# Optimization experiments

Measured on AMD Instinct MI355X. Metric: run time of the kernel, lower is better.

Reference implementation:

```python
import jax, jax.numpy as jnp
import numpy as np

SR = 8                      # search_range
MO = 2 * SR + 1             # max_offset = 17
NC = MO * MO                # 289 cost-volume channels


def _l2_normalize(x, eps=1e-12):
    # torch F.normalize(p=2, dim=1): x / max(||x||_2, eps)
    n = jnp.sqrt(jnp.sum(x * x, axis=1, keepdims=True))
    return x / jnp.maximum(n, eps)


def _conv2d(x, w, b, pad, groups=1):
    out = jax.lax.conv_general_dilated(
        x, w, window_strides=(1, 1), padding=[(pad, pad), (pad, pad)],
        feature_group_count=groups,
        dimension_numbers=('NCHW', 'OIHW', 'NCHW'))
    return out + b[None, :, None, None]


def _cost_volume(x1, x2, sr, norm_both=False):
    x1 = _l2_normalize(x1)
    if norm_both:
        x2 = _l2_normalize(x2)
    bs, c, h, w = x1.shape
    padded = jnp.pad(x2, ((0, 0), (0, 0), (sr, sr), (sr, sr)))
    mo = 2 * sr + 1
    # offsets in (j outer, i inner) order, matching the original double loop
    jj, ii = jnp.meshgrid(jnp.arange(mo), jnp.arange(mo), indexing='ij')
    offs = jnp.stack([jj.reshape(-1), ii.reshape(-1)], axis=-1)  # [mo^2, 2]

    def step(carry, off):
        sl = jax.lax.dynamic_slice(padded, (0, 0, off[0], off[1]), (bs, c, h, w))
        return carry, jnp.mean(x1 * sl, axis=1)  # [bs, h, w]

    _, cv = jax.lax.scan(step, None, offs)       # [mo^2, bs, h, w]
    cv = jnp.transpose(cv, (1, 0, 2, 3))          # [bs, mo^2, h, w]
    return jax.nn.leaky_relu(cv, 0.1)


def setup_inputs() -> dict:
    key = jax.random.key(0)
    ks = jax.random.split(key, 8)
    bs, c, h, w = 4, 256, 64, 64
    scale = 0.05
    return {
        'f1': jax.random.normal(ks[0], (bs, c, h, w), jnp.float32),
        'f2': jax.random.normal(ks[1], (bs, c, h, w), jnp.float32),
        'att_w': jax.random.normal(ks[2], (NC, 1, 7, 7), jnp.float32) * scale,
        'att_b': jax.random.normal(ks[3], (NC,), jnp.float32) * scale,
        'agg1_w': jax.random.normal(ks[4], (NC // 2, NC, 3, 3), jnp.float32) * scale,
        'agg1_b': jax.random.normal(ks[5], (NC // 2,), jnp.float32) * scale,
        'agg2_w': jax.random.normal(ks[6], (49, NC // 2, 3, 3), jnp.float32) * scale,
        'agg2_b': jax.random.normal(ks[7], (49,), jnp.float32) * scale,
    }


def reference(f1, f2, att_w, att_b, agg1_w, agg1_b, agg2_w, agg2_b):
    match_vol = _cost_volume(f1, f2, SR, norm_both=False)          # [bs,289,h,w]
    att = _conv2d(match_vol, att_w, att_b, pad=3, groups=NC)       # depthwise 7x7
    att_vol = match_vol * att
    h1 = jax.nn.relu(_conv2d(att_vol, agg1_w, agg1_b, pad=1))      # Conv(289->144,3)
    out = jax.nn.relu(_conv2d(h1, agg2_w, agg2_b, pad=1))          # Conv(144->49,3)
    return out
```

## Files before the change

### kernel.cpp

```cpp
#include <hip/hip_runtime.h>
#include <hip/hip_bf16.h>

#define BS   4
#define C    256
#define HW   4096
#define NPIX 16384
#define NCH  289
#define MO   17
#define PH   80
#define PW   80
#define C1   144
#define C2   49
#define ASTR 264
#define ICP  320
#define IC3  192
#define CVP  70
#define CVC  320
#define CH64 72

typedef __bf16  bf16x8 __attribute__((ext_vector_type(8)));
typedef float   f32x4  __attribute__((ext_vector_type(4)));
typedef unsigned short us8 __attribute__((ext_vector_type(8)));

__device__ __forceinline__ void halo_zero_dev(unsigned short* p, int H, int halo,
                                              int Cc, int blk, int t) {
    int W = H;
    int inter = H - 2 * halo;
    int total_pos = H * W - inter * inter;
    int chunks = Cc >> 3;
    size_t tot = (size_t)total_pos * chunks * BS;
    size_t idx = (size_t)blk * 256 + t;
    if (idx >= tot) return;
    int c8 = (int)(idx % chunks);
    size_t r = idx / chunks;
    int pos = (int)(r % total_pos);
    int b = (int)(r / total_pos);
    int h, w;
    int topbot = 2 * halo * W;
    if (pos < halo * W) { h = pos / W; w = pos % W; }
    else if (pos < topbot) { int q = pos - halo * W; h = H - halo + q / W; w = q % W; }
    else {
        int q = pos - topbot;
        int row = q / (2 * halo), off = q % (2 * halo);
        h = halo + row;
        w = (off < halo) ? off : (W - 2 * halo + off);
    }
    us8 z = {0, 0, 0, 0, 0, 0, 0, 0};
    *(us8*)&p[(((size_t)b * H + h) * W + w) * Cc + c8 * 8] = z;
}

__global__ void setup_kernel(unsigned short* __restrict__ x2bf, unsigned short* __restrict__ cvp,
                             unsigned short* __restrict__ avp, unsigned short* __restrict__ h1p,
                             const float* __restrict__ w1, unsigned short* __restrict__ wb1,
                             const float* __restrict__ w2, unsigned short* __restrict__ wb2,
                             const float* __restrict__ att_w, float* __restrict__ wdwp,
                             const float* __restrict__ f1, unsigned short* __restrict__ x1bf,
                             const float* __restrict__ f2) {
    __shared__ float shmem[16 * 257 + 16];
    int blk = blockIdx.x;
    int t = threadIdx.x;
    if (blk < 4030) {
        if (blk < 1152) { halo_zero_dev(x2bf, PH, 8, C, blk, t); return; }
        if (blk < 1655) { halo_zero_dev(cvp, CVP, 3, CVC, blk - 1152, t); return; }
        if (blk < 1818) { halo_zero_dev(avp, 66, 1, ICP, blk - 1655, t); return; }
        if (blk < 1916) { halo_zero_dev(h1p, 66, 1, IC3, blk - 1818, t); return; }
        if (blk < 3536) {
            int idx = (blk - 1916) * 256 + t;
            int tap = idx / (C1 * ICP);
            int r = idx - tap * (C1 * ICP);
            int oc = r / ICP;
            int ic = r - oc * ICP;
            float v = (ic < NCH) ? w1[((size_t)(oc * NCH + ic)) * 9 + tap] : 0.f;
            __hip_bfloat16 hb = __float2bfloat16(v);
            wb1[idx] = *(unsigned short*)&hb;
            return;
        }
        if (blk < 3968) {
            int idx = (blk - 3536) * 256 + t;
            int tap = idx / (64 * IC3);
            int r = idx - tap * (64 * IC3);
            int oc = r / IC3;
            int ic = r - oc * IC3;
            float v = (oc < C2 && ic < C1) ? w2[((size_t)(oc * C1 + ic)) * 9 + tap] : 0.f;
            __hip_bfloat16 hb = __float2bfloat16(v);
            wb2[idx] = *(unsigned short*)&hb;
            return;
        }
        {
            int idx = (blk - 3968) * 256 + t;
            if (idx >= 49 * CVC) return;
            int tap = idx / CVC;
            int ch = idx - tap * CVC;
            wdwp[idx] = (ch < NCH) ? att_w[ch * 49 + tap] : 0.f;
        }
        return;
    }
    if (blk < 5054) {
        float* tileT = shmem;
        float* invS = shmem + 16 * 257;
        int bb = blk - 4030;
        int pblk = bb & 255, b = bb >> 8;
        int p0 = pblk * 16;
        int tx = t & 15, ty = t >> 4;
        const float* s = f1 + (size_t)b * C * HW;
#pragma unroll
        for (int i2 = 0; i2 < 16; ++i2) {
            int c = ty + 16 * i2;
            tileT[tx * 257 + c] = s[(size_t)c * HW + p0 + tx];
        }
        __syncthreads();
        int px = t >> 4;
        int l = t & 15;
        float ssum = 0.f;
#pragma unroll
        for (int j2 = 0; j2 < 16; ++j2) {
            float v = tileT[px * 257 + l + 16 * j2];
            ssum += v * v;
        }
        ssum += __shfl_xor(ssum, 1);
        ssum += __shfl_xor(ssum, 2);
        ssum += __shfl_xor(ssum, 4);
        ssum += __shfl_xor(ssum, 8);
        if (l == 0) invS[px] = 1.0f / fmaxf(sqrtf(ssum), 1e-12f);
        __syncthreads();
#pragma unroll 4
        for (int p = 0; p < 16; ++p) {
            float v = tileT[p * 257 + t] * invS[p];
            __hip_bfloat16 hb = __float2bfloat16(v);
            x1bf[((size_t)b * HW + p0 + p) * C + t] = *(unsigned short*)&hb;
        }
        return;
    }
    {
        float* tile = shmem;
        int bb = blk - 5054;
        int pblk = bb & 127;
        int cblk = (bb >> 7) & 7;
        int b    = bb >> 10;
        int tx = t & 31, ty = t >> 5;
        int c0 = cblk * 32, p0 = pblk * 32;
        const float* s = f2 + (size_t)b * C * HW;
#pragma unroll
        for (int i = 0; i < 4; ++i) {
            int c = c0 + ty + 8 * i;
            tile[(ty + 8 * i) * 33 + tx] = s[(size_t)c * HW + p0 + tx];
        }
        __syncthreads();
#pragma unroll
        for (int i = 0; i < 4; ++i) {
            int p = p0 + ty + 8 * i;
            float v = tile[tx * 33 + ty + 8 * i];
            int c = c0 + tx;
            int h = p >> 6, w = p & 63;
            __hip_bfloat16 hb = __float2bfloat16(v);
            x2bf[(((size_t)b * PH + h + 8) * PW + (w + 8)) * C + c] = *(unsigned short*)&hb;
        }
    }
}

__global__ __launch_bounds__(512, 2)
void cv_mfma_kernel(const unsigned short* __restrict__ x1b,
                    const unsigned short* __restrict__ x2b,
                    unsigned short* __restrict__ cvp) {
    __shared__ __align__(16) unsigned short x2s[2][32 * ASTR];
    int i = blockIdx.x;
    int xcd = i & 7;
    int j = i >> 3;
    int hp = xcd * 2 + (j & 1);
    int jj = j >> 1;
    int wseg = jj & 3;
    int b = jj >> 2;
    int h0 = hp * 4;
    int w0 = wseg * 16;
    int t = threadIdx.x;
    int wave = t >> 6, lane = t & 63;
    int lrow = lane & 15, quad = lane >> 4;
    int row_w = wave >> 1, ct = wave & 1;
    int h = h0 + row_w;
    int col_l = ct * 16 + lrow;

    const unsigned short* x1p = x1b + ((size_t)b * HW + h * 64 + w0) * C;
    bf16x8 a[8];
#pragma unroll
    for (int kk = 0; kk < 8; ++kk)
        a[kk] = *(const bf16x8*)&x1p[(size_t)lrow * C + kk * 32 + quad * 8];

    const unsigned short* x2base = x2b + (size_t)b * PH * PW * C;

    {
        const unsigned short* rowp = x2base + ((size_t)h0 * PW + w0) * C;
#pragma unroll
        for (int s = 0; s < 2; ++s) {
            int v = t + s * 512;
            int col = v >> 5, ch8 = v & 31;
            *(us8*)&x2s[0][col * ASTR + ch8 * 8] = *(const us8*)&rowp[(size_t)col * C + ch8 * 8];
        }
    }
    __syncthreads();

    for (int rr = 0; rr < 20; ++rr) {
        us8 pr[2];
        bool dop = (rr + 1 < 20);
        if (dop) {
            const unsigned short* rowp = x2base + ((size_t)(h0 + rr + 1) * PW + w0) * C;
#pragma unroll
            for (int s = 0; s < 2; ++s) {
                int v = t + s * 512;
                int col = v >> 5, ch8 = v & 31;
                pr[s] = *(const us8*)&rowp[(size_t)col * C + ch8 * 8];
            }
        }

        int dj = rr - row_w;
        if ((unsigned)dj <= 16u) {
            const unsigned short* xs = x2s[rr & 1];
            f32x4 acc = {0.f, 0.f, 0.f, 0.f};
#pragma unroll
            for (int kk = 0; kk < 8; ++kk) {
                bf16x8 bb = *(const bf16x8*)&xs[col_l * ASTR + kk * 32 + quad * 8];
                acc = __builtin_amdgcn_mfma_f32_16x16x32_bf16(a[kk], bb, acc, 0, 0, 0);
            }
#pragma unroll
            for (int r = 0; r < 4; ++r) {
                int px_l = quad * 4 + r;
                int di = col_l - px_l;
                if ((unsigned)di <= 16u) {
                    float v = acc[r] * (1.0f / 256.0f);
                    v = (v > 0.f) ? v : 0.1f * v;
                    __hip_bfloat16 hb = __float2bfloat16(v);
                    cvp[(((size_t)b * CVP + h + 3) * CVP + (w0 + px_l + 3)) * CVC + dj * MO + di] =
                        *(unsigned short*)&hb;
                }
            }
        }

        if (dop) {
            unsigned short* dst = x2s[(rr + 1) & 1];
#pragma unroll
            for (int s = 0; s < 2; ++s) {
                int v = t + s * 512;
                int col = v >> 5, ch8 = v & 31;
                *(us8*)&dst[col * ASTR + ch8 * 8] = pr[s];
            }
            __syncthreads();
        }
    }
}

__global__ __launch_bounds__(256, 4)
void dw_att_tiled(const unsigned short* __restrict__ cvp,
                  const float* __restrict__ wdwp,
                  const float* __restrict__ att_b, unsigned short* __restrict__ av_pad) {
    __shared__ __align__(16) unsigned short actS[14 * 14 * 64];
    __shared__ float wdwS[49 * 64];
    int i = blockIdx.x;
    int ty = i & 7;
    int j = i >> 3;
    int cc = j % 5;
    int rest = j / 5;
    int tx = rest & 7, b = rest >> 3;
    int x0 = tx * 8, y0 = ty * 8;
    int c0 = cc * 64;
    int t = threadIdx.x;

    const unsigned short* cvb = cvp + (((size_t)b * CVP + y0) * CVP + x0) * CVC + c0;
    for (int v = t; v < 14 * 14 * 8; v += 256) {
        int rc = v >> 3, c8v = v & 7;
        int yy = rc / 14, xx = rc - yy * 14;
        *(us8*)&actS[rc * 64 + c8v * 8] =
            *(const us8*)&cvb[((size_t)yy * CVP + xx) * CVC + c8v * 8];
    }
    for (int v = t; v < 49 * 64; v += 256) {
        int tap = v >> 6, ch = v & 63;
        wdwS[v] = wdwp[tap * CVC + c0 + ch];
    }
    __syncthreads();

    int pr2 = t & 31;
    int rowg = t >> 5;
    int chl0 = 2 * pr2;
    int ch0 = c0 + chl0;
    float bv0 = (ch0 < NCH) ? att_b[ch0] : 0.f;
    float bv1 = (ch0 + 1 < NCH) ? att_b[ch0 + 1] : 0.f;
    float acc0[8], acc1[8];
#pragma unroll
    for (int px = 0; px < 8; ++px) { acc0[px] = bv0; acc1[px] = bv1; }

    for (int dy = 0; dy < 7; ++dy) {
        float w0[7], w1[7];
#pragma unroll
        for (int dx = 0; dx < 7; ++dx) {
            float2 wv = *(const float2*)&wdwS[(dy * 7 + dx) * 64 + chl0];
            w0[dx] = wv.x; w1[dx] = wv.y;
        }
        int row = rowg + dy;
        float r0[14], r1[14];
#pragma unroll
        for (int xx = 0; xx < 14; ++xx) {
            unsigned u = *(const unsigned*)&actS[(row * 14 + xx) * 64 + chl0];
            r0[xx] = __uint_as_float(u << 16);
            r1[xx] = __uint_as_float(u & 0xffff0000u);
        }
#pragma unroll
        for (int dx = 0; dx < 7; ++dx)
#pragma unroll
            for (int px = 0; px < 8; ++px) {
                acc0[px] += r0[px + dx] * w0[dx];
                acc1[px] += r1[px + dx] * w1[dx];
            }
    }

    if (ch0 < NCH) {
        bool pair = (ch0 + 1 < NCH);
#pragma unroll
        for (int px = 0; px < 8; ++px) {
            unsigned u = *(const unsigned*)&actS[((rowg + 3) * 14 + (px + 3)) * 64 + chl0];
            float c0v = __uint_as_float(u << 16);
            float c1v = __uint_as_float(u & 0xffff0000u);
            __hip_bfloat16 h0 = __float2bfloat16(c0v * acc0[px]);
            __hip_bfloat16 h1 = __float2bfloat16(c1v * acc1[px]);
            size_t o = (((size_t)b * 66 + y0 + rowg + 1) * 66 + (x0 + px + 1)) * ICP + ch0;
            if (pair) {
                unsigned ov = ((unsigned)*(unsigned short*)&h1 << 16) | (unsigned)*(unsigned short*)&h0;
                *(unsigned*)&av_pad[o] = ov;
            } else {
                av_pad[o] = *(unsigned short*)&h0;
            }
        }
    }
}

__global__ void agg1_mfma_kernel(const unsigned short* __restrict__ av_pad,
                                 const unsigned short* __restrict__ wb1,
                                 const float* __restrict__ bias,
                                 unsigned short* __restrict__ h1p) {
    __shared__ __align__(16) unsigned short aS2[2][66 * CH64];
    int i = blockIdx.x;
    int xcd = i & 7;
    int j = i >> 3;
    int h = xcd * 8 + (j & 7);
    int b = j >> 3;
    int t = threadIdx.x;
    int wave = t >> 6, lane = t & 63;
    int lrow = lane & 15, quad = lane >> 4;
    int ot0 = (wave == 0) ? 0 : (wave * 2 + 1);
    int nt  = (wave == 0) ? 3 : 2;

    f32x4 acc[4][3];
#pragma unroll
    for (int m = 0; m < 4; ++m)
#pragma unroll
        for (int ii = 0; ii < 3; ++ii) acc[m][ii] = (f32x4){0.f, 0.f, 0.f, 0.f};

    const unsigned short* avb = av_pad + (((size_t)b * 66 + h) * 66) * ICP;

    {
        const unsigned short* arow = avb;
        *(us8*)&aS2[0][(t >> 3) * CH64 + (t & 7) * 8] =
            *(const us8*)&arow[(size_t)(t >> 3) * ICP + (t & 7) * 8];
        {
            int v = t + 256;
            *(us8*)&aS2[0][(v >> 3) * CH64 + (v & 7) * 8] =
                *(const us8*)&arow[(size_t)(v >> 3) * ICP + (v & 7) * 8];
        }
        if (t < 16) {
            int v = t + 512;
            *(us8*)&aS2[0][(v >> 3) * CH64 + (v & 7) * 8] =
                *(const us8*)&arow[(size_t)(v >> 3) * ICP + (v & 7) * 8];
        }
    }
    bf16x8 bcur[3][2], bnxt[3][2];
#pragma unroll
    for (int ii = 0; ii < 3; ++ii)
        if (ii < nt)
#pragma unroll
            for (int c2 = 0; c2 < 2; ++c2)
                bcur[ii][c2] = *(const bf16x8*)&wb1[((size_t)((ot0 + ii) * 16 + lrow)) * ICP +
                                                    c2 * 32 + quad * 8];
    __syncthreads();

    for (int p2 = 0; p2 < 15; ++p2) {
        int dy = p2 / 5, cc = p2 % 5;
        us8 ar0, ar1, ar2;
        bool doA = (p2 + 1 < 15);
        if (doA) {
            int dyn = (p2 + 1) / 5, ccn = (p2 + 1) % 5;
            const unsigned short* arow = avb + (size_t)dyn * 66 * ICP + ccn * 64;
            ar0 = *(const us8*)&arow[(size_t)(t >> 3) * ICP + (t & 7) * 8];
            {
                int v = t + 256;
                ar1 = *(const us8*)&arow[(size_t)(v >> 3) * ICP + (v & 7) * 8];
            }
            if (t < 16) {
                int v = t + 512;
                ar2 = *(const us8*)&arow[(size_t)(v >> 3) * ICP + (v & 7) * 8];
            }
        }
        const unsigned short* aP = aS2[p2 & 1];
#pragma unroll
        for (int dx = 0; dx < 3; ++dx) {
            bool doB = !(p2 == 14 && dx == 2);
            if (doB) {
                int tapn, ccb;
                if (dx < 2) { tapn = dy * 3 + dx + 1; ccb = cc; }
                else { tapn = ((p2 + 1) / 5) * 3; ccb = (p2 + 1) % 5; }
                const unsigned short* wt = wb1 + ((size_t)tapn * C1 + lrow) * ICP +
                                           ccb * 64 + quad * 8;
#pragma unroll
                for (int ii = 0; ii < 3; ++ii)
                    if (ii < nt)
#pragma unroll
                        for (int c2 = 0; c2 < 2; ++c2)
                            bnxt[ii][c2] = *(const bf16x8*)&wt[(size_t)((ot0 + ii) * 16) * ICP +
                                                               c2 * 32];
            }
#pragma unroll
            for (int c2 = 0; c2 < 2; ++c2) {
#pragma unroll
                for (int m = 0; m < 4; ++m) {
                    bf16x8 af = *(const bf16x8*)&aP[(m * 16 + lrow + dx) * CH64 + c2 * 32 + quad * 8];
#pragma unroll
                    for (int ii = 0; ii < 3; ++ii)
                        if (ii < nt)
                            acc[m][ii] = __builtin_amdgcn_mfma_f32_16x16x32_bf16(af, bcur[ii][c2],
                                                                                 acc[m][ii], 0, 0, 0);
                }
            }
            if (doB) {
#pragma unroll
                for (int ii = 0; ii < 3; ++ii)
#pragma unroll
                    for (int c2 = 0; c2 < 2; ++c2)
                        bcur[ii][c2] = bnxt[ii][c2];
            }
        }
        if (doA) {
            unsigned short* dst = aS2[(p2 + 1) & 1];
            *(us8*)&dst[(t >> 3) * CH64 + (t & 7) * 8] = ar0;
            {
                int v = t + 256;
                *(us8*)&dst[(v >> 3) * CH64 + (v & 7) * 8] = ar1;
            }
            if (t < 16) {
                int v = t + 512;
                *(us8*)&dst[(v >> 3) * CH64 + (v & 7) * 8] = ar2;
            }
            __syncthreads();
        }
    }

    size_t rowbase = ((size_t)b * 66 + h + 1) * 66;
#pragma unroll
    for (int m = 0; m < 4; ++m)
#pragma unroll
        for (int ii = 0; ii < 3; ++ii)
            if (ii < nt) {
                int oc = (ot0 + ii) * 16 + lrow;
                float bv = bias[oc];
#pragma unroll
                for (int r = 0; r < 4; ++r) {
                    int w = m * 16 + quad * 4 + r;
                    float val = fmaxf(acc[m][ii][r] + bv, 0.f);
                    __hip_bfloat16 hb = __float2bfloat16(val);
                    h1p[(rowbase + (w + 1)) * IC3 + oc] = *(unsigned short*)&hb;
                }
            }
}

__global__ void agg2_mfma_kernel(const unsigned short* __restrict__ h1p,
                                 const unsigned short* __restrict__ wb2,
                                 const float* __restrict__ bias, float* __restrict__ out) {
    __shared__ __align__(16) unsigned short aS2[2][66 * CH64];
    int i = blockIdx.x;
    int xcd = i & 7;
    int j = i >> 3;
    int h = xcd * 8 + (j & 7);
    int b = j >> 3;
    int t = threadIdx.x;
    int wave = t >> 6, lane = t & 63;
    int lrow = lane & 15, quad = lane >> 4;
    int pt = wave;

    f32x4 acc[4];
#pragma unroll
    for (int ot = 0; ot < 4; ++ot) acc[ot] = (f32x4){0.f, 0.f, 0.f, 0.f};

    const unsigned short* h1b = h1p + (((size_t)b * 66 + h) * 66) * IC3;

    {
        *(us8*)&aS2[0][(t >> 3) * CH64 + (t & 7) * 8] =
            *(const us8*)&h1b[(size_t)(t >> 3) * IC3 + (t & 7) * 8];
        {
            int v = t + 256;
            *(us8*)&aS2[0][(v >> 3) * CH64 + (v & 7) * 8] =
                *(const us8*)&h1b[(size_t)(v >> 3) * IC3 + (v & 7) * 8];
        }
        if (t < 16) {
            int v = t + 512;
            *(us8*)&aS2[0][(v >> 3) * CH64 + (v & 7) * 8] =
                *(const us8*)&h1b[(size_t)(v >> 3) * IC3 + (v & 7) * 8];
        }
    }
    bf16x8 bcur[4][2], bnxt[4][2];
#pragma unroll
    for (int ot = 0; ot < 4; ++ot)
#pragma unroll
        for (int c2 = 0; c2 < 2; ++c2)
            bcur[ot][c2] = *(const bf16x8*)&wb2[((size_t)(ot * 16 + lrow)) * IC3 +
                                                c2 * 32 + quad * 8];
    __syncthreads();

    for (int p2 = 0; p2 < 9; ++p2) {
        int dy = p2 / 3, cc = p2 % 3;
        us8 ar0, ar1, ar2;
        bool doA = (p2 + 1 < 9);
        if (doA) {
            int dyn = (p2 + 1) / 3, ccn = (p2 + 1) % 3;
            const unsigned short* arow = h1b + (size_t)dyn * 66 * IC3 + ccn * 64;
            ar0 = *(const us8*)&arow[(size_t)(t >> 3) * IC3 + (t & 7) * 8];
            {
                int v = t + 256;
                ar1 = *(const us8*)&arow[(size_t)(v >> 3) * IC3 + (v & 7) * 8];
            }
            if (t < 16) {
                int v = t + 512;
                ar2 = *(const us8*)&arow[(size_t)(v >> 3) * IC3 + (v & 7) * 8];
            }
        }
        const unsigned short* aP = aS2[p2 & 1];
#pragma unroll
        for (int dx = 0; dx < 3; ++dx) {
            bool doB = !(p2 == 8 && dx == 2);
            if (doB) {
                int tapn, ccb;
                if (dx < 2) { tapn = dy * 3 + dx + 1; ccb = cc; }
                else { tapn = ((p2 + 1) / 3) * 3; ccb = (p2 + 1) % 3; }
                const unsigned short* wt = wb2 + ((size_t)tapn * 64 + lrow) * IC3 +
                                           ccb * 64 + quad * 8;
#pragma unroll
                for (int ot = 0; ot < 4; ++ot)
#pragma unroll
                    for (int c2 = 0; c2 < 2; ++c2)
                        bnxt[ot][c2] = *(const bf16x8*)&wt[(size_t)(ot * 16) * IC3 + c2 * 32];
            }
#pragma unroll
            for (int c2 = 0; c2 < 2; ++c2) {
                bf16x8 af = *(const bf16x8*)&aP[(pt * 16 + lrow + dx) * CH64 + c2 * 32 + quad * 8];
#pragma unroll
                for (int ot = 0; ot < 4; ++ot)
                    acc[ot] = __builtin_amdgcn_mfma_f32_16x16x32_bf16(af, bcur[ot][c2],
                                                                      acc[ot], 0, 0, 0);
            }
            if (doB) {
#pragma unroll
                for (int ot = 0; ot < 4; ++ot)
#pragma unroll
                    for (int c2 = 0; c2 < 2; ++c2)
                        bcur[ot][c2] = bnxt[ot][c2];
            }
        }
        if (doA) {
            unsigned short* dst = aS2[(p2 + 1) & 1];
            *(us8*)&dst[(t >> 3) * CH64 + (t & 7) * 8] = ar0;
            {
                int v = t + 256;
                *(us8*)&dst[(v >> 3) * CH64 + (v & 7) * 8] = ar1;
            }
            if (t < 16) {
                int v = t + 512;
                *(us8*)&dst[(v >> 3) * CH64 + (v & 7) * 8] = ar2;
            }
            __syncthreads();
        }
    }

#pragma unroll
    for (int ot = 0; ot < 4; ++ot) {
        int o = ot * 16 + lrow;
        if (o < C2) {
            float bv = bias[o];
#pragma unroll
            for (int r = 0; r < 4; ++r) {
                int w = pt * 16 + quad * 4 + r;
                out[((size_t)b * C2 + o) * HW + h * 64 + w] = fmaxf(acc[ot][r] + bv, 0.f);
            }
        }
    }
}

extern "C" void kernel_launch(void* const* d_in, const int* in_sizes, int n_in,
                              void* d_out, int out_size, void* d_ws, size_t ws_size,
                              hipStream_t stream) {
    const float* f1    = (const float*)d_in[0];
    const float* f2    = (const float*)d_in[1];
    const float* att_w = (const float*)d_in[2];
    const float* att_b = (const float*)d_in[3];
    const float* w1    = (const float*)d_in[4];
    const float* b1    = (const float*)d_in[5];
    const float* w2    = (const float*)d_in[6];
    const float* b2    = (const float*)d_in[7];
    float* out = (float*)d_out;

    char* wsb = (char*)d_ws;
    size_t off = 0;
    float* wdwp = (float*)(wsb + off); off += (size_t)49 * CVC * 4;
    off = (off + 15) & ~(size_t)15;
    unsigned short* x1bf = (unsigned short*)(wsb + off); off += (size_t)NPIX * C * 2;
    unsigned short* x2bf = (unsigned short*)(wsb + off); off += (size_t)BS * PH * PW * C * 2;
    unsigned short* cvp  = (unsigned short*)(wsb + off); off += (size_t)BS * CVP * CVP * CVC * 2;
    unsigned short* avp  = (unsigned short*)(wsb + off); off += (size_t)BS * 66 * 66 * ICP * 2;
    unsigned short* wb1  = (unsigned short*)(wsb + off); off += (size_t)9 * C1 * ICP * 2;
    unsigned short* h1p  = (unsigned short*)(wsb + off); off += (size_t)BS * 66 * 66 * IC3 * 2;
    unsigned short* wb2  = (unsigned short*)(wsb + off); off += (size_t)9 * 64 * IC3 * 2;
    if (ws_size < off) return;

    setup_kernel<<<9150, 256, 0, stream>>>(x2bf, cvp, avp, h1p, w1, wb1, w2, wb2,
                                           att_w, wdwp, f1, x1bf, f2);
    cv_mfma_kernel<<<256, 512, 0, stream>>>(x1bf, x2bf, cvp);
    dw_att_tiled<<<1280, 256, 0, stream>>>(cvp, wdwp, att_b, avp);
    agg1_mfma_kernel<<<256, 256, 0, stream>>>(avp, wb1, b1, h1p);
    agg2_mfma_kernel<<<256, 256, 0, stream>>>(h1p, wb2, b2, out);
}
```

Baseline: 205.7 us.

## Stage conv weights through double-buffered LDS and split agg1 across eight waves

Both aggregation conv kernels now stage weight tiles through double-buffered shared memory per (tap, channel-chunk) step, instead of having each wave read weight fragments directly from global memory. agg1 doubles its block size to 512 threads, with waves split over output-channel groups and pixel halves, so each wave holds fewer accumulators. The aim is to cut redundant global weight traffic and raise latency hiding. The cost is a barrier every step (45 and 27 steps) instead of one per input-row chunk, plus more LDS use per block.

```diff
diff --git a/kernel.cpp b/kernel.cpp
--- a/kernel.cpp
+++ b/kernel.cpp
@@ -330,11 +330,28 @@
     }
 }
 
-__global__ void agg1_mfma_kernel(const unsigned short* __restrict__ av_pad,
-                                 const unsigned short* __restrict__ wb1,
-                                 const float* __restrict__ bias,
-                                 unsigned short* __restrict__ h1p) {
+__device__ __forceinline__ const unsigned short* b1ptr(const unsigned short* wb1, int m) {
+    int dy = m / 15, rm = m % 15, cc = rm / 3, dx = rm % 3;
+    return wb1 + ((size_t)(dy * 3 + dx) * C1) * ICP + cc * 64;
+}
+
+#define A1_BLOAD(S0, S1, S2, P)                                                      \
+    S0 = *(const us8*)&(P)[(size_t)(t >> 3) * ICP + (t & 7) * 8];                    \
+    { int v_ = t + 512; S1 = *(const us8*)&(P)[(size_t)(v_ >> 3) * ICP + (v_ & 7) * 8]; } \
+    if (t < 128) { int v_ = t + 1024; S2 = *(const us8*)&(P)[(size_t)(v_ >> 3) * ICP + (v_ & 7) * 8]; }
+
+#define A1_BWRITE(S0, S1, S2, D)                                                     \
+    *(us8*)&(D)[(t >> 3) * CH64 + (t & 7) * 8] = S0;                                 \
+    { int v_ = t + 512; *(us8*)&(D)[(v_ >> 3) * CH64 + (v_ & 7) * 8] = S1; }         \
+    if (t < 128) { int v_ = t + 1024; *(us8*)&(D)[(v_ >> 3) * CH64 + (v_ & 7) * 8] = S2; }
+
+__global__ __launch_bounds__(512, 2)
+void agg1_mfma_kernel(const unsigned short* __restrict__ av_pad,
+                      const unsigned short* __restrict__ wb1,
+                      const float* __restrict__ bias,
+                      unsigned short* __restrict__ h1p) {
     __shared__ __align__(16) unsigned short aS2[2][66 * CH64];
+    __shared__ __align__(16) unsigned short bS[2][C1 * CH64];
     int i = blockIdx.x;
     int xcd = i & 7;
     int j = i >> 3;
@@ -343,107 +360,73 @@
     int t = threadIdx.x;
     int wave = t >> 6, lane = t & 63;
     int lrow = lane & 15, quad = lane >> 4;
-    int ot0 = (wave == 0) ? 0 : (wave * 2 + 1);
-    int nt  = (wave == 0) ? 3 : 2;
-
-    f32x4 acc[4][3];
-#pragma unroll
-    for (int m = 0; m < 4; ++m)
+    int og = wave & 3, mg = wave >> 2;
+    int ot0 = (og == 0) ? 0 : (og * 2 + 1);
+    int nt  = (og == 0) ? 3 : 2;
+
+    f32x4 acc[2][3];
+#pragma unroll
+    for (int m = 0; m < 2; ++m)
 #pragma unroll
         for (int ii = 0; ii < 3; ++ii) acc[m][ii] = (f32x4){0.f, 0.f, 0.f, 0.f};
 
     const unsigned short* avb = av_pad + (((size_t)b * 66 + h) * 66) * ICP;
 
+    us8 bE0, bE1, bE2, bO0, bO1, bO2;
+    us8 a0, a1;
+
     {
-        const unsigned short* arow = avb;
-        *(us8*)&aS2[0][(t >> 3) * CH64 + (t & 7) * 8] =
-            *(const us8*)&arow[(size_t)(t >> 3) * ICP + (t & 7) * 8];
-        {
-            int v = t + 256;
-            *(us8*)&aS2[0][(v >> 3) * CH64 + (v & 7) * 8] =
-                *(const us8*)&arow[(size_t)(v >> 3) * ICP + (v & 7) * 8];
-        }
-        if (t < 16) {
-            int v = t + 512;
-            *(us8*)&aS2[0][(v >> 3) * CH64 + (v & 7) * 8] =
-                *(const us8*)&arow[(size_t)(v >> 3) * ICP + (v & 7) * 8];
-        }
-    }
-    bf16x8 bcur[3][2], bnxt[3][2];
-#pragma unroll
-    for (int ii = 0; ii < 3; ++ii)
-        if (ii < nt)
-#pragma unroll
-            for (int c2 = 0; c2 < 2; ++c2)
-                bcur[ii][c2] = *(const bf16x8*)&wb1[((size_t)((ot0 + ii) * 16 + lrow)) * ICP +
-                                                    c2 * 32 + quad * 8];
+        us8 p0, p1, p2, q0, q1;
+        const unsigned short* w0p = b1ptr(wb1, 0);
+        A1_BLOAD(p0, p1, p2, w0p)
+        q0 = *(const us8*)&avb[(size_t)(t >> 3) * ICP + (t & 7) * 8];
+        if (t < 16) { int v_ = t + 512; q1 = *(const us8*)&avb[(size_t)(v_ >> 3) * ICP + (v_ & 7) * 8]; }
+        A1_BLOAD(bO0, bO1, bO2, b1ptr(wb1, 1))
+        A1_BWRITE(p0, p1, p2, bS[0])
+        *(us8*)&aS2[0][(t >> 3) * CH64 + (t & 7) * 8] = q0;
+        if (t < 16) { int v_ = t + 512; *(us8*)&aS2[0][(v_ >> 3) * CH64 + (v_ & 7) * 8] = q1; }
+    }
     __syncthreads();
 
-    for (int p2 = 0; p2 < 15; ++p2) {
-        int dy = p2 / 5, cc = p2 % 5;
-        us8 ar0, ar1, ar2;
-        bool doA = (p2 + 1 < 15);
-        if (doA) {
-            int dyn = (p2 + 1) / 5, ccn = (p2 + 1) % 5;
-            const unsigned short* arow = avb + (size_t)dyn * 66 * ICP + ccn * 64;
-            ar0 = *(const us8*)&arow[(size_t)(t >> 3) * ICP + (t & 7) * 8];
-            {
-                int v = t + 256;
-                ar1 = *(const us8*)&arow[(size_t)(v >> 3) * ICP + (v & 7) * 8];
-            }
-            if (t < 16) {
-                int v = t + 512;
-                ar2 = *(const us8*)&arow[(size_t)(v >> 3) * ICP + (v & 7) * 8];
-            }
-        }
-        const unsigned short* aP = aS2[p2 & 1];
-#pragma unroll
-        for (int dx = 0; dx < 3; ++dx) {
-            bool doB = !(p2 == 14 && dx == 2);
-            if (doB) {
-                int tapn, ccb;
-                if (dx < 2) { tapn = dy * 3 + dx + 1; ccb = cc; }
-                else { tapn = ((p2 + 1) / 5) * 3; ccb = (p2 + 1) % 5; }
-                const unsigned short* wt = wb1 + ((size_t)tapn * C1 + lrow) * ICP +
-                                           ccb * 64 + quad * 8;
+    for (int k = 0; k < 45; ++k) {
+        int dx = k % 3;
+        if (k < 43) {
+            const unsigned short* wt = b1ptr(wb1, k + 2);
+            if ((k & 1) == 0) { A1_BLOAD(bE0, bE1, bE2, wt) }
+            else              { A1_BLOAD(bO0, bO1, bO2, wt) }
+        }
+        if (dx == 0 && k < 42) {
+            int p = k / 3 + 1;
+            const unsigned short* ar = avb + (size_t)(p / 5) * 66 * ICP + (p % 5) * 64;
+            a0 = *(const us8*)&ar[(size_t)(t >> 3) * ICP + (t & 7) * 8];
+            if (t < 16) { int v_ = t + 512; a1 = *(const us8*)&ar[(size_t)(v_ >> 3) * ICP + (v_ & 7) * 8]; }
+        }
+        const unsigned short* aP = aS2[(k / 3) & 1];
+        const unsigned short* bP = bS[k & 1];
+#pragma unroll
+        for (int c2 = 0; c2 < 2; ++c2) {
+            bf16x8 bfr[3];
+#pragma unroll
+            for (int ii = 0; ii < 3; ++ii)
+                if (ii < nt)
+                    bfr[ii] = *(const bf16x8*)&bP[((ot0 + ii) * 16 + lrow) * CH64 + c2 * 32 + quad * 8];
+#pragma unroll
+            for (int m = 0; m < 2; ++m) {
+                bf16x8 af = *(const bf16x8*)&aP[((mg * 2 + m) * 16 + lrow + dx) * CH64 + c2 * 32 + quad * 8];
 #pragma unroll
                 for (int ii = 0; ii < 3; ++ii)
                     if (ii < nt)
-#pragma unroll
-                        for (int c2 = 0; c2 < 2; ++c2)
-                            bnxt[ii][c2] = *(const bf16x8*)&wt[(size_t)((ot0 + ii) * 16) * ICP +
-                                                               c2 * 32];
-            }
-#pragma unroll
-            for (int c2 = 0; c2 < 2; ++c2) {
-#pragma unroll
-                for (int m = 0; m < 4; ++m) {
-                    bf16x8 af = *(const bf16x8*)&aP[(m * 16 + lrow + dx) * CH64 + c2 * 32 + quad * 8];
-#pragma unroll
-                    for (int ii = 0; ii < 3; ++ii)
-                        if (ii < nt)
-                            acc[m][ii] = __builtin_amdgcn_mfma_f32_16x16x32_bf16(af, bcur[ii][c2],
-                                                                                 acc[m][ii], 0, 0, 0);
-                }
-            }
-            if (doB) {
-#pragma unroll
-                for (int ii = 0; ii < 3; ++ii)
-#pragma unroll
-                    for (int c2 = 0; c2 < 2; ++c2)
-                        bcur[ii][c2] = bnxt[ii][c2];
-            }
-        }
-        if (doA) {
-            unsigned short* dst = aS2[(p2 + 1) & 1];
-            *(us8*)&dst[(t >> 3) * CH64 + (t & 7) * 8] = ar0;
-            {
-                int v = t + 256;
-                *(us8*)&dst[(v >> 3) * CH64 + (v & 7) * 8] = ar1;
-            }
-            if (t < 16) {
-                int v = t + 512;
-                *(us8*)&dst[(v >> 3) * CH64 + (v & 7) * 8] = ar2;
+                        acc[m][ii] = __builtin_amdgcn_mfma_f32_16x16x32_bf16(af, bfr[ii], acc[m][ii], 0, 0, 0);
+            }
+        }
+        if (k < 44) {
+            unsigned short* dst = bS[(k + 1) & 1];
+            if (((k + 1) & 1) == 0) { A1_BWRITE(bE0, bE1, bE2, dst) }
+            else                    { A1_BWRITE(bO0, bO1, bO2, dst) }
+            if (dx == 2) {
+                unsigned short* adst = aS2[(k / 3 + 1) & 1];
+                *(us8*)&adst[(t >> 3) * CH64 + (t & 7) * 8] = a0;
+                if (t < 16) { int v_ = t + 512; *(us8*)&adst[(v_ >> 3) * CH64 + (v_ & 7) * 8] = a1; }
             }
             __syncthreads();
         }
@@ -451,7 +434,7 @@
 
     size_t rowbase = ((size_t)b * 66 + h + 1) * 66;
 #pragma unroll
-    for (int m = 0; m < 4; ++m)
+    for (int m = 0; m < 2; ++m)
 #pragma unroll
         for (int ii = 0; ii < 3; ++ii)
             if (ii < nt) {
@@ -459,18 +442,33 @@
                 float bv = bias[oc];
 #pragma unroll
                 for (int r = 0; r < 4; ++r) {
-                    int w = m * 16 + quad * 4 + r;
+                    int wl = (mg * 2 + m) * 16 + quad * 4 + r;
                     float val = fmaxf(acc[m][ii][r] + bv, 0.f);
                     __hip_bfloat16 hb = __float2bfloat16(val);
-                    h1p[(rowbase + (w + 1)) * IC3 + oc] = *(unsigned short*)&hb;
+                    h1p[(rowbase + (wl + 1)) * IC3 + oc] = *(unsigned short*)&hb;
                 }
             }
 }
 
-__global__ void agg2_mfma_kernel(const unsigned short* __restrict__ h1p,
-                                 const unsigned short* __restrict__ wb2,
-                                 const float* __restrict__ bias, float* __restrict__ out) {
+__device__ __forceinline__ const unsigned short* b2ptr(const unsigned short* wb2, int m) {
+    int dy = m / 9, rm = m % 9, cc = rm / 3, dx = rm % 3;
+    return wb2 + ((size_t)(dy * 3 + dx) * 64) * IC3 + cc * 64;
+}
+
+#define A2_BLOAD(S0, S1, P)                                                          \
+    S0 = *(const us8*)&(P)[(size_t)(t >> 3) * IC3 + (t & 7) * 8];                    \
+    { int v_ = t + 256; S1 = *(const us8*)&(P)[(size_t)(v_ >> 3) * IC3 + (v_ & 7) * 8]; }
+
+#define A2_BWRITE(S0, S1, D)                                                         \
+    *(us8*)&(D)[(t >> 3) * CH64 + (t & 7) * 8] = S0;                                 \
+    { int v_ = t + 256; *(us8*)&(D)[(v_ >> 3) * CH64 + (v_ & 7) * 8] = S1; }
+
+__global__ __launch_bounds__(256, 1)
+void agg2_mfma_kernel(const unsigned short* __restrict__ h1p,
+                      const unsigned short* __restrict__ wb2,
+                      const float* __restrict__ bias, float* __restrict__ out) {
     __shared__ __align__(16) unsigned short aS2[2][66 * CH64];
+    __shared__ __align__(16) unsigned short bS2[2][64 * CH64];
     int i = blockIdx.x;
     int xcd = i & 7;
     int j = i >> 3;
@@ -487,88 +485,57 @@
 
     const unsigned short* h1b = h1p + (((size_t)b * 66 + h) * 66) * IC3;
 
+    us8 bE0, bE1, bO0, bO1;
+    us8 a0, a1, a2;
+
     {
-        *(us8*)&aS2[0][(t >> 3) * CH64 + (t & 7) * 8] =
-            *(const us8*)&h1b[(size_t)(t >> 3) * IC3 + (t & 7) * 8];
-        {
-            int v = t + 256;
-            *(us8*)&aS2[0][(v >> 3) * CH64 + (v & 7) * 8] =
-                *(const us8*)&h1b[(size_t)(v >> 3) * IC3 + (v & 7) * 8];
-        }
-        if (t < 16) {
-            int v = t + 512;
-            *(us8*)&aS2[0][(v >> 3) * CH64 + (v & 7) * 8] =
-                *(const us8*)&h1b[(size_t)(v >> 3) * IC3 + (v & 7) * 8];
-        }
-    }
-    bf16x8 bcur[4][2], bnxt[4][2];
-#pragma unroll
-    for (int ot = 0; ot < 4; ++ot)
-#pragma unroll
-        for (int c2 = 0; c2 < 2; ++c2)
-            bcur[ot][c2] = *(const bf16x8*)&wb2[((size_t)(ot * 16 + lrow)) * IC3 +
-                                                c2 * 32 + quad * 8];
+        us8 p0, p1, q0, q1, q2;
+        A2_BLOAD(p0, p1, wb2)
+        q0 = *(const us8*)&h1b[(size_t)(t >> 3) * IC3 + (t & 7) * 8];
+        { int v_ = t + 256; q1 = *(const us8*)&h1b[(size_t)(v_ >> 3) * IC3 + (v_ & 7) * 8]; }
+        if (t < 16) { int v_ = t + 512; q2 = *(const us8*)&h1b[(size_t)(v_ >> 3) * IC3 + (v_ & 7) * 8]; }
+        A2_BLOAD(bO0, bO1, b2ptr(wb2, 1))
+        A2_BWRITE(p0, p1, bS2[0])
+        *(us8*)&aS2[0][(t >> 3) * CH64 + (t & 7) * 8] = q0;
+        { int v_ = t + 256; *(us8*)&aS2[0][(v_ >> 3) * CH64 + (v_ & 7) * 8] = q1; }
+        if (t < 16) { int v_ = t + 512; *(us8*)&aS2[0][(v_ >> 3) * CH64 + (v_ & 7) * 8] = q2; }
+    }
     __syncthreads();
 
-    for (int p2 = 0; p2 < 9; ++p2) {
-        int dy = p2 / 3, cc = p2 % 3;
-        us8 ar0, ar1, ar2;
-        bool doA = (p2 + 1 < 9);
-        if (doA) {
-            int dyn = (p2 + 1) / 3, ccn = (p2 + 1) % 3;
-            const unsigned short* arow = h1b + (size_t)dyn * 66 * IC3 + ccn * 64;
-            ar0 = *(const us8*)&arow[(size_t)(t >> 3) * IC3 + (t & 7) * 8];
-            {
-                int v = t + 256;
-                ar1 = *(const us8*)&arow[(size_t)(v >> 3) * IC3 + (v & 7) * 8];
-            }
-            if (t < 16) {
-                int v = t + 512;
-                ar2 = *(const us8*)&arow[(size_t)(v >> 3) * IC3 + (v & 7) * 8];
-            }
-        }
-        const unsigned short* aP = aS2[p2 & 1];
-#pragma unroll
-        for (int dx = 0; dx < 3; ++dx) {
-            bool doB = !(p2 == 8 && dx == 2);
-            if (doB) {
-                int tapn, ccb;
-                if (dx < 2) { tapn = dy * 3 + dx + 1; ccb = cc; }
-                else { tapn = ((p2 + 1) / 3) * 3; ccb = (p2 + 1) % 3; }
-                const unsigned short* wt = wb2 + ((size_t)tapn * 64 + lrow) * IC3 +
-                                           ccb * 64 + quad * 8;
-#pragma unroll
-                for (int ot = 0; ot < 4; ++ot)
-#pragma unroll
-                    for (int c2 = 0; c2 < 2; ++c2)
-                        bnxt[ot][c2] = *(const bf16x8*)&wt[(size_t)(ot * 16) * IC3 + c2 * 32];
-            }
-#pragma unroll
-            for (int c2 = 0; c2 < 2; ++c2) {
-                bf16x8 af = *(const bf16x8*)&aP[(pt * 16 + lrow + dx) * CH64 + c2 * 32 + quad * 8];
-#pragma unroll
-                for (int ot = 0; ot < 4; ++ot)
-                    acc[ot] = __builtin_amdgcn_mfma_f32_16x16x32_bf16(af, bcur[ot][c2],
-                                                                      acc[ot], 0, 0, 0);
-            }
-            if (doB) {
-#pragma unroll
-                for (int ot = 0; ot < 4; ++ot)
-#pragma unroll
-                    for (int c2 = 0; c2 < 2; ++c2)
-                        bcur[ot][c2] = bnxt[ot][c2];
-            }
-        }
-        if (doA) {
-            unsigned short* dst = aS2[(p2 + 1) & 1];
-            *(us8*)&dst[(t >> 3) * CH64 + (t & 7) * 8] = ar0;
-            {
-                int v = t + 256;
-                *(us8*)&dst[(v >> 3) * CH64 + (v & 7) * 8] = ar1;
-            }
-            if (t < 16) {
-                int v = t + 512;
-                *(us8*)&dst[(v >> 3) * CH64 + (v & 7) * 8] = ar2;
+    for (int k = 0; k < 27; ++k) {
+        int dx = k % 3;
+        if (k < 25) {
+            const unsigned short* wt = b2ptr(wb2, k + 2);
+            if ((k & 1) == 0) { A2_BLOAD(bE0, bE1, wt) }
+            else              { A2_BLOAD(bO0, bO1, wt) }
+        }
+        if (dx == 0 && k < 24) {
+            int p = k / 3 + 1;
+            const unsigned short* ar = h1b + (size_t)(p / 3) * 66 * IC3 + (p % 3) * 64;
+            a0 = *(const us8*)&ar[(size_t)(t >> 3) * IC3 + (t & 7) * 8];
+            { int v_ = t + 256; a1 = *(const us8*)&ar[(size_t)(v_ >> 3) * IC3 + (v_ & 7) * 8]; }
+            if (t < 16) { int v_ = t + 512; a2 = *(const us8*)&ar[(size_t)(v_ >> 3) * IC3 + (v_ & 7) * 8]; }
+        }
+        const unsigned short* aP = aS2[(k / 3) & 1];
+        const unsigned short* bP = bS2[k & 1];
+#pragma unroll
+        for (int c2 = 0; c2 < 2; ++c2) {
+            bf16x8 af = *(const bf16x8*)&aP[(pt * 16 + lrow + dx) * CH64 + c2 * 32 + quad * 8];
+#pragma unroll
+            for (int ot = 0; ot < 4; ++ot) {
+                bf16x8 bfr = *(const bf16x8*)&bP[(ot * 16 + lrow) * CH64 + c2 * 32 + quad * 8];
+                acc[ot] = __builtin_amdgcn_mfma_f32_16x16x32_bf16(af, bfr, acc[ot], 0, 0, 0);
+            }
+        }
+        if (k < 26) {
+            unsigned short* dst = bS2[(k + 1) & 1];
+            if (((k + 1) & 1) == 0) { A2_BWRITE(bE0, bE1, dst) }
+            else                    { A2_BWRITE(bO0, bO1, dst) }
+            if (dx == 2) {
+                unsigned short* adst = aS2[(k / 3 + 1) & 1];
+                *(us8*)&adst[(t >> 3) * CH64 + (t & 7) * 8] = a0;
+                { int v_ = t + 256; *(us8*)&adst[(v_ >> 3) * CH64 + (v_ & 7) * 8] = a1; }
+                if (t < 16) { int v_ = t + 512; *(us8*)&adst[(v_ >> 3) * CH64 + (v_ & 7) * 8] = a2; }
             }
             __syncthreads();
         }
@@ -618,6 +585,6 @@
                                            att_w, wdwp, f1, x1bf, f2);
     cv_mfma_kernel<<<256, 512, 0, stream>>>(x1bf, x2bf, cvp);
     dw_att_tiled<<<1280, 256, 0, stream>>>(cvp, wdwp, att_b, avp);
-    agg1_mfma_kernel<<<256, 256, 0, stream>>>(avp, wb1, b1, h1p);
+    agg1_mfma_kernel<<<256, 512, 0, stream>>>(avp, wb1, b1, h1p);
     agg2_mfma_kernel<<<256, 256, 0, stream>>>(h1p, wb2, b2, out);
 }
```

Result: faster. 190.0 us (-7.6%).
